# Optimization experiments

Measured on AMD Instinct MI355X. Metric: run time of the kernel, lower is better.

## Reference

```python
import jax, jax.numpy as jnp
import numpy as np
from jax.ops import segment_sum

GRID = 32        # cells per axis; offset grid is (GRID+1)^3
T = 48           # number of accepted MC topologies
N_PTS = 131072

# 12 cube edges: base (lower) corner offset and axis the edge runs along.
# e0..3: x/y edges of z=0 face, e4..7: same at z=1, e8..11: vertical z edges.
EDGE_BASE = np.array([[0,0,0],[1,0,0],[0,1,0],[0,0,0],
                      [0,0,1],[1,0,1],[0,1,1],[0,0,1],
                      [0,0,0],[1,0,0],[1,1,0],[0,1,0]], dtype=np.int32)
EDGE_AXIS = np.array([0,1,0,1, 0,1,0,1, 2,2,2,2], dtype=np.int32)
EDGE_DIR  = np.eye(3, dtype=np.float32)[EDGE_AXIS]          # [12,3] unit dirs


def _dot(u, v):
    return jnp.sum(u * v, axis=-1)


def _safe_div(n, d, eps=1e-12):
    return n / jnp.where(jnp.abs(d) > eps, d, eps)


def _point_tri_dist_sq(p, a, b, c):
    """Squared distance from p to triangle (a,b,c); Ericson closest-point
    algorithm with full vertex/edge/interior region clamping, vectorized.
    p broadcasts against a/b/c over leading dims; last dim is xyz."""
    ab = b - a; ac = c - a; ap = p - a
    d1 = _dot(ab, ap); d2 = _dot(ac, ap)
    bp = p - b; d3 = _dot(ab, bp); d4 = _dot(ac, bp)
    cp = p - c; d5 = _dot(ab, cp); d6 = _dot(ac, cp)
    vc = d1 * d4 - d3 * d2
    vb = d5 * d2 - d1 * d6
    va = d3 * d6 - d5 * d4
    v_ab = _safe_div(d1, d1 - d3)
    w_ac = _safe_div(d2, d2 - d6)
    w_bc = _safe_div(d4 - d3, (d4 - d3) + (d5 - d6))
    inv = _safe_div(jnp.ones_like(va), va + vb + vc)
    v_in = vb * inv; w_in = vc * inv
    q = a + ab * v_in[..., None] + ac * w_in[..., None]                      # interior
    q = jnp.where(((va <= 0) & ((d4 - d3) >= 0) & ((d5 - d6) >= 0))[..., None],
                  b + (c - b) * w_bc[..., None], q)                          # edge BC
    q = jnp.where(((vb <= 0) & (d2 >= 0) & (d6 <= 0))[..., None],
                  a + ac * w_ac[..., None], q)                               # edge AC
    q = jnp.where(((d6 >= 0) & (d5 <= d6))[..., None], c, q)                 # vertex C
    q = jnp.where(((vc <= 0) & (d1 >= 0) & (d3 <= 0))[..., None],
                  a + ab * v_ab[..., None], q)                               # edge AB
    q = jnp.where(((d3 >= 0) & (d4 <= d3))[..., None], b, q)                 # vertex B
    q = jnp.where(((d1 <= 0) & (d2 <= 0))[..., None], a, q)                  # vertex A
    diff = p - q
    return _dot(diff, diff)


def setup_inputs() -> dict:
    key = jax.random.key(0)
    k1, k2, k3 = jax.random.split(key, 3)
    offset = jax.random.uniform(k1, (3, GRID + 1, GRID + 1, GRID + 1), dtype=jnp.float32)
    points = jax.random.uniform(k2, (N_PTS, 3), dtype=jnp.float32) * GRID
    tri_table = jax.random.randint(k3, (T, 3, 3), 0, 12, dtype=jnp.int32)
    return {"offset": offset, "points": points, "tri_table": tri_table}


def reference(offset, points, tri_table):
    edge_base_i = jnp.asarray(EDGE_BASE)                 # [12,3] int
    edge_base_f = jnp.asarray(EDGE_BASE, dtype=offset.dtype)
    edge_dir = jnp.asarray(EDGE_DIR, dtype=offset.dtype)
    edge_axis = jnp.asarray(EDGE_AXIS)

    cell = jnp.clip(jnp.floor(points).astype(jnp.int32), 0, GRID - 1)   # [N,3]
    local = points - cell.astype(points.dtype)                          # [N,3] in [0,1)^3

    # grid index of each edge's base corner -> edge offset parameter t in [0,1]
    gidx = cell[:, None, :] + edge_base_i[None, :, :]                   # [N,12,3]
    t = offset[edge_axis[None, :], gidx[..., 0], gidx[..., 1], gidx[..., 2]]  # [N,12]
    verts = edge_base_f[None] + edge_dir[None] * t[..., None]           # [N,12,3] local coords

    tri = verts[:, tri_table]                                           # [N,T,3tri,3vert,3]
    a = tri[:, :, :, 0, :]; b = tri[:, :, :, 1, :]; c = tri[:, :, :, 2, :]
    p = local[:, None, None, :]                                         # [N,1,1,3]
    d2 = _point_tri_dist_sq(p, a, b, c)                                 # [N,T,3]
    d_min = jnp.min(d2, axis=-1)                                        # [N,T]

    cell_id = (cell[:, 0] * GRID + cell[:, 1]) * GRID + cell[:, 2]      # [N]
    distances_full = segment_sum(d_min, cell_id, num_segments=GRID ** 3)  # [GRID^3, T]
    return distances_full
```

## Files before the change

kernel.cpp:

```cpp
#include <hip/hip_runtime.h>

#define GRID 32
#define NT 48
#define BLK 256
#define SPLIT 16
#define PPB (BLK / SPLIT)
#define NCELLS (GRID * GRID * GRID)
#define CAP 32
#define CAP2 16
#define GSTRIDE 148

#define EDGE_PACK ( (0ULL<<0) | (9ULL<<5) | (2ULL<<10) | (8ULL<<15) | \
                    (4ULL<<20) | (13ULL<<25) | (6ULL<<30) | (12ULL<<35) | \
                    (16ULL<<40) | (17ULL<<45) | (19ULL<<50) | (18ULL<<55) )

__device__ __forceinline__ float tri_dist_gram(float AA, float AB, float AC,
                                               float BB, float BC, float CC) {
    float d1 = AA - AB, d2 = AA - AC;
    float d3 = AB - BB, d4 = AB - BC;
    float d5 = AC - BC, d6 = AC - CC;
    float d43 = BB - BC;
    float d56 = CC - BC;
    float vc = d1 * d4 - d3 * d2;
    float vb = d5 * d2 - d1 * d6;
    float va = d3 * d6 - d5 * d4;

    bool cbc = (va <= 0.f) & (d43 >= 0.f) & (d56 >= 0.f);
    bool cac = (vb <= 0.f) & (d2 >= 0.f) & (d6 <= 0.f);
    bool ccc = (d6 >= 0.f) & (d5 <= d6);
    bool cab = (vc <= 0.f) & (d1 >= 0.f) & (d3 <= 0.f);
    bool cbb = (d3 >= 0.f) & (d4 <= d3);
    bool caa = (d1 <= 0.f) & (d2 <= 0.f);

    float nv = vb, nw = vc, den = va + vb + vc;
    nw = cbc ? d43 : nw;  den = cbc ? d43 + d56 : den;
    nv = cac ? 0.f : nv;  nw = cac ? d2  : nw;  den = cac ? d2 - d6 : den;
    nv = cab ? d1  : nv;  nw = cab ? 0.f : nw;  den = cab ? d1 - d3 : den;
    bool mode = cbc & !cac & !cab;

    float dd  = (fabsf(den) > 1e-12f) ? den : 1e-12f;
    float inv = __builtin_amdgcn_rcpf(dd);
    float vp = nv * inv;
    float wp = nw * inv;
    float u = mode ? 0.f : 1.f - vp - wp;
    float v = mode ? 1.f - wp : vp;
    float e1 = fmaf(AC, wp, fmaf(AB, v, AA * u));
    float e2 = fmaf(BC, wp, fmaf(BB, v, AB * u));
    float e3 = fmaf(CC, wp, fmaf(BC, v, AC * u));
    float r  = fmaf(wp, e3, fmaf(v, e2, u * e1));
    r = (ccc & !cab) ? CC : r;
    r = cbb ? BB : r;
    r = caa ? AA : r;
    return r;
}

template<bool SLOT>
__global__ __launch_bounds__(BLK, 8) void eval_kernel(
    const float* __restrict__ offset,
    const float* __restrict__ points,
    const int*   __restrict__ tri_table,
    int*         __restrict__ cnt,
    int*         __restrict__ wlist,
    int*         __restrict__ ovf_cnt,
    int*         __restrict__ ovf,
    float*       __restrict__ dmin,
    float*       __restrict__ dmin_ovf,
    int n)
{
    __shared__ float4 v_s[PPB * 13];
    __shared__ float  gram[PPB * GSTRIDE];
    __shared__ int2   goff[NT * 3];
    __shared__ int    pos_s[PPB];

    const int tid = threadIdx.x;
    const int g   = blockIdx.x * BLK + tid;
    const int pt  = g >> 4;
    const int grp = tid & 15;
    const int pl  = tid >> 4;
    const bool active = (pt < n);

    if (tid < NT * 3) {
        int i = tri_table[tid * 3 + 0];
        int j = tri_table[tid * 3 + 1];
        int k = tri_table[tid * 3 + 2];
        int o0 = (i * 13) | ((i * 12 + j) << 8) | ((i * 12 + k) << 16);
        int o1 = (j * 13) | ((j * 12 + k) << 8) | ((k * 13) << 16);
        goff[tid] = make_int2(o0, o1);
    }

    float4 vi = make_float4(0.f, 0.f, 0.f, 0.f);
    if (active) {
        float px = points[pt * 3 + 0];
        float py = points[pt * 3 + 1];
        float pz = points[pt * 3 + 2];
        int cx = min(max((int)floorf(px), 0), GRID - 1);
        int cy = min(max((int)floorf(py), 0), GRID - 1);
        int cz = min(max((int)floorf(pz), 0), GRID - 1);
        if (grp == 0) {
            int cellid = ((cx * GRID) + cy) * GRID + cz;
            int pos = atomicAdd(&cnt[cellid], 1);
            if (SLOT) {
                int base;
                if (pos < CAP2) base = cellid * CAP2 + pos;
                else { int e = atomicAdd(ovf_cnt, 1); ovf[e] = cellid;
                       base = 0x40000000 | e; }
                pos_s[pl] = base;
            } else {
                if (pos < CAP) wlist[cellid * CAP + pos] = pt;
                else { int e = atomicAdd(ovf_cnt, 1); ovf[e] = (cellid << 17) | pt; }
            }
        }
        if (grp < 12) {
            float lx = px - (float)cx;
            float ly = py - (float)cy;
            float lz = pz - (float)cz;
            unsigned nib = (unsigned)(EDGE_PACK >> (5 * grp)) & 31u;
            int gx = cx + (int)(nib & 1u);
            int gy = cy + (int)((nib >> 1) & 1u);
            int gz = cz + (int)((nib >> 2) & 1u);
            int ax = (int)(nib >> 3);
            float t = offset[((ax * 33 + gx) * 33 + gy) * 33 + gz];
            float vx = (ax == 0) ? t : (float)(nib & 1u);
            float vy = (ax == 1) ? t : (float)((nib >> 1) & 1u);
            float vz = (ax == 2) ? t : (float)((nib >> 2) & 1u);
            vi = make_float4(lx - vx, ly - vy, lz - vz, 0.0f);
            v_s[pl * 13 + grp] = vi;
        }
    }
    __syncthreads();
    if (active && grp < 12) {
        float* gp = &gram[pl * GSTRIDE];
        int j = grp;
#pragma unroll
        for (int d = 0; d < 7; d++) {
            float4 vj = v_s[pl * 13 + j];
            float dv = fmaf(vi.z, vj.z, fmaf(vi.y, vj.y, vi.x * vj.x));
            gp[grp * 12 + j] = dv;
            gp[j * 12 + grp] = dv;
            j = (j == 11) ? 0 : j + 1;
        }
    }
    __syncthreads();
    if (!active) return;

    const float* gp = &gram[pl * GSTRIDE];
    const int2* gofft = &goff[grp * 9];
    float dm[3];
#pragma unroll
    for (int r = 0; r < 3; r++) {
        int2 oa = gofft[r * 3 + 0];
        int2 ob = gofft[r * 3 + 1];
        int2 oc = gofft[r * 3 + 2];
        float a0 = gp[oa.x & 255], a1 = gp[(oa.x >> 8) & 255], a2 = gp[(unsigned)oa.x >> 16];
        float a3 = gp[oa.y & 255], a4 = gp[(oa.y >> 8) & 255], a5 = gp[(unsigned)oa.y >> 16];
        float b0 = gp[ob.x & 255], b1 = gp[(ob.x >> 8) & 255], b2 = gp[(unsigned)ob.x >> 16];
        float b3 = gp[ob.y & 255], b4 = gp[(ob.y >> 8) & 255], b5 = gp[(unsigned)ob.y >> 16];
        float c0 = gp[oc.x & 255], c1 = gp[(oc.x >> 8) & 255], c2 = gp[(unsigned)oc.x >> 16];
        float c3 = gp[oc.y & 255], c4 = gp[(oc.y >> 8) & 255], c5 = gp[(unsigned)oc.y >> 16];
        float d0 = tri_dist_gram(a0, a1, a2, a3, a4, a5);
        float d1 = tri_dist_gram(b0, b1, b2, b3, b4, b5);
        float d2 = tri_dist_gram(c0, c1, c2, c3, c4, c5);
        dm[r] = fminf(fminf(d0, d1), d2);
    }
    float* dp;
    if (SLOT) {
        int base = pos_s[pl];
        dp = (base & 0x40000000)
               ? &dmin_ovf[(size_t)(base & 0x3FFFFFFF) * NT + grp * 3]
               : &dmin[(size_t)base * NT + grp * 3];
    } else {
        dp = &dmin[(size_t)pt * NT + grp * 3];
    }
    dp[0] = dm[0]; dp[1] = dm[1]; dp[2] = dm[2];
}

__global__ __launch_bounds__(BLK) void reduce_slot_kernel(
    const int*   __restrict__ cnt,
    const int*   __restrict__ ovf_cnt,
    const int*   __restrict__ ovf,
    const float* __restrict__ dmin,
    const float* __restrict__ dmin_ovf,
    float*       __restrict__ out)
{
    const int tid  = threadIdx.x;
    const int grp  = tid & 15;
    const int pl   = tid >> 4;
    const int cell = blockIdx.x * PPB + pl;

    const int c = min(cnt[cell], CAP2);
    const float* bp = &dmin[(size_t)cell * CAP2 * NT + grp * 3];
    float s0 = 0.f, s1 = 0.f, s2 = 0.f;
    for (int i = 0; i < c; i++) {
        s0 += bp[0]; s1 += bp[1]; s2 += bp[2];
        bp += NT;
    }
    const int movf = *ovf_cnt;
    for (int e = 0; e < movf; e++) {
        if (ovf[e] == cell) {
            const float* dp = &dmin_ovf[(size_t)e * NT + grp * 3];
            s0 += dp[0]; s1 += dp[1]; s2 += dp[2];
        }
    }
    float* op = &out[cell * NT + grp * 3];
    op[0] = s0; op[1] = s1; op[2] = s2;
}

__global__ __launch_bounds__(BLK) void reduce_kernel(
    const int*   __restrict__ cnt,
    const int*   __restrict__ wlist,
    const int*   __restrict__ ovf_cnt,
    const int*   __restrict__ ovf,
    const float* __restrict__ dmin,
    float*       __restrict__ out)
{
    const int tid  = threadIdx.x;
    const int grp  = tid & 15;
    const int pl   = tid >> 4;
    const int cell = blockIdx.x * PPB + pl;

    const int c = min(cnt[cell], CAP);
    const int* wl = &wlist[cell * CAP];
    float s0 = 0.f, s1 = 0.f, s2 = 0.f;
    for (int i = 0; i < c; i++) {
        int pt = wl[i];
        const float* dp = &dmin[(size_t)pt * NT + grp * 3];
        s0 += dp[0]; s1 += dp[1]; s2 += dp[2];
    }
    const int movf = *ovf_cnt;
    for (int e = 0; e < movf; e++) {
        int v = ovf[e];
        if ((v >> 17) == cell) {
            int pt = v & 0x1FFFF;
            const float* dp = &dmin[(size_t)pt * NT + grp * 3];
            s0 += dp[0]; s1 += dp[1]; s2 += dp[2];
        }
    }
    float* op = &out[cell * NT + grp * 3];
    op[0] = s0; op[1] = s1; op[2] = s2;
}

__global__ __launch_bounds__(BLK) void ptd_kernel(
    const float* __restrict__ offset,
    const float* __restrict__ points,
    const int*   __restrict__ tri_table,
    float*       __restrict__ out,
    int n)
{
    __shared__ float4 v_s[PPB * 13];
    __shared__ float  gram[PPB * GSTRIDE];
    __shared__ int2   goff[NT * 3];

    const int tid = threadIdx.x;
    const int g   = blockIdx.x * BLK + tid;
    const int pt  = g >> 4;
    const int grp = tid & 15;
    const int pl  = tid >> 4;
    const bool active = (pt < n);

    if (tid < NT * 3) {
        int i = tri_table[tid * 3 + 0];
        int j = tri_table[tid * 3 + 1];
        int k = tri_table[tid * 3 + 2];
        int o0 = (i * 13) | ((i * 12 + j) << 8) | ((i * 12 + k) << 16);
        int o1 = (j * 13) | ((j * 12 + k) << 8) | ((k * 13) << 16);
        goff[tid] = make_int2(o0, o1);
    }

    float4 vi = make_float4(0.f, 0.f, 0.f, 0.f);
    int cx = 0, cy = 0, cz = 0;
    if (active) {
        float px = points[pt * 3 + 0];
        float py = points[pt * 3 + 1];
        float pz = points[pt * 3 + 2];
        cx = min(max((int)floorf(px), 0), GRID - 1);
        cy = min(max((int)floorf(py), 0), GRID - 1);
        cz = min(max((int)floorf(pz), 0), GRID - 1);
        if (grp < 12) {
            float lx = px - (float)cx;
            float ly = py - (float)cy;
            float lz = pz - (float)cz;
            unsigned nib = (unsigned)(EDGE_PACK >> (5 * grp)) & 31u;
            int gx = cx + (int)(nib & 1u);
            int gy = cy + (int)((nib >> 1) & 1u);
            int gz = cz + (int)((nib >> 2) & 1u);
            int ax = (int)(nib >> 3);
            float t = offset[((ax * 33 + gx) * 33 + gy) * 33 + gz];
            float vx = (ax == 0) ? t : (float)(nib & 1u);
            float vy = (ax == 1) ? t : (float)((nib >> 1) & 1u);
            float vz = (ax == 2) ? t : (float)((nib >> 2) & 1u);
            vi = make_float4(lx - vx, ly - vy, lz - vz, 0.0f);
            v_s[pl * 13 + grp] = vi;
        }
    }
    __syncthreads();
    if (active && grp < 12) {
        float* gp = &gram[pl * GSTRIDE];
        int j = grp;
#pragma unroll
        for (int d = 0; d < 7; d++) {
            float4 vj = v_s[pl * 13 + j];
            float dv = fmaf(vi.z, vj.z, fmaf(vi.y, vj.y, vi.x * vj.x));
            gp[grp * 12 + j] = dv;
            gp[j * 12 + grp] = dv;
            j = (j == 11) ? 0 : j + 1;
        }
    }
    __syncthreads();
    if (!active) return;

    const float* gp = &gram[pl * GSTRIDE];
    float* outp = out + ((((cx * GRID) + cy) * GRID + cz) * NT);
    const int2* gofft = &goff[grp * 9];
#pragma unroll
    for (int r = 0; r < 3; r++) {
        float dmn;
#pragma unroll
        for (int k = 0; k < 3; k++) {
            int2 o = gofft[r * 3 + k];
            float AA = gp[o.x & 255];
            float AB = gp[(o.x >> 8) & 255];
            float AC = gp[(unsigned)o.x >> 16];
            float BB = gp[o.y & 255];
            float BC = gp[(o.y >> 8) & 255];
            float CC = gp[(unsigned)o.y >> 16];
            float d = tri_dist_gram(AA, AB, AC, BB, BC, CC);
            dmn = (k == 0) ? d : fminf(dmn, d);
        }
        atomicAdd(&outp[grp * 3 + r], dmn);
    }
}

extern "C" void kernel_launch(void* const* d_in, const int* in_sizes, int n_in,
                              void* d_out, int out_size, void* d_ws, size_t ws_size,
                              hipStream_t stream) {
    const float* offset    = (const float*)d_in[0];
    const float* points    = (const float*)d_in[1];
    const int*   tri_table = (const int*)d_in[2];
    float* out = (float*)d_out;
    int n = in_sizes[1] / 3;

    const size_t CNT_BYTES = (size_t)NCELLS * 4;
    const size_t OVFC_OFF  = CNT_BYTES;
    const size_t OVF_OFF   = CNT_BYTES + 128;
    const size_t TAIL_OFF  = (OVF_OFF + (size_t)n * 4 + 255) & ~(size_t)255;

    const size_t DMIN2_BYTES = (size_t)NCELLS * CAP2 * NT * 4;
    const size_t DOVF_OFF    = TAIL_OFF + DMIN2_BYTES;
    const size_t WS_SLOT     = DOVF_OFF + (size_t)n * NT * 4;

    const size_t WL_BYTES = (size_t)NCELLS * CAP * 4;
    const size_t DMIN_OFF = TAIL_OFF + WL_BYTES;
    const size_t WS_FB    = DMIN_OFF + (size_t)n * NT * 4;

    char* ws = (char*)d_ws;
    int* cnt     = (int*)(ws);
    int* ovf_cnt = (int*)(ws + OVFC_OFF);
    int* ovf     = (int*)(ws + OVF_OFF);

    long total = (long)n * SPLIT;
    int blocks = (int)((total + BLK - 1) / BLK);

    if (ws_size >= WS_SLOT) {
        float* dmin2    = (float*)(ws + TAIL_OFF);
        float* dmin_ovf = (float*)(ws + DOVF_OFF);
        hipMemsetAsync(ws, 0, OVF_OFF, stream);
        eval_kernel<true><<<blocks, BLK, 0, stream>>>(
            offset, points, tri_table, cnt, nullptr, ovf_cnt, ovf,
            dmin2, dmin_ovf, n);
        reduce_slot_kernel<<<NCELLS / PPB, BLK, 0, stream>>>(
            cnt, ovf_cnt, ovf, dmin2, dmin_ovf, out);
    } else if (ws_size >= WS_FB) {
        int*   wlist = (int*)(ws + TAIL_OFF);
        float* dmin  = (float*)(ws + DMIN_OFF);
        hipMemsetAsync(ws, 0, OVF_OFF, stream);
        eval_kernel<false><<<blocks, BLK, 0, stream>>>(
            offset, points, tri_table, cnt, wlist, ovf_cnt, ovf,
            dmin, nullptr, n);
        reduce_kernel<<<NCELLS / PPB, BLK, 0, stream>>>(
            cnt, wlist, ovf_cnt, ovf, dmin, out);
    } else {
        hipMemsetAsync(d_out, 0, (size_t)out_size * sizeof(float), stream);
        ptd_kernel<<<blocks, BLK, 0, stream>>>(offset, points, tri_table, out, n);
    }
}
```

Measured before the change: 112.6 us.

## Pack Gram matrix as float2 pairs to halve LDS reads per triangle

Stores the per-point Gram matrix interleaved as (G[i][j], G[j][j]) float2 pairs so each triangle needs three 8-byte LDS reads instead of six scalar reads. The offset table is repacked into one int per triangle and read as int4 rows. The aim is to cut LDS load instruction count in the hot evaluation loop. In exchange the shared-memory footprint roughly doubles and launch_bounds drops from 8 to 6 blocks, which may lower occupancy.

Result: no change. 112.3 us (-0.3%).

```diff
diff --git a/kernel.cpp b/kernel.cpp
--- a/kernel.cpp
+++ b/kernel.cpp
@@ -8,7 +8,10 @@
 #define NCELLS (GRID * GRID * GRID)
 #define CAP 32
 #define CAP2 16
-#define GSTRIDE 148
+#define GSTRIDE 144
+#define G2F 290
+
+typedef float f32x2 __attribute__((ext_vector_type(2)));
 
 #define EDGE_PACK ( (0ULL<<0) | (9ULL<<5) | (2ULL<<10) | (8ULL<<15) | \
                     (4ULL<<20) | (13ULL<<25) | (6ULL<<30) | (12ULL<<35) | \
@@ -54,8 +57,22 @@
     return r;
 }
 
+__device__ __forceinline__ float eval_one(const f32x2* gp2, int o) {
+    f32x2 pij = gp2[o & 255];
+    f32x2 pjk = gp2[(o >> 8) & 255];
+    f32x2 pki = gp2[(unsigned)o >> 16];
+    return tri_dist_gram(pij.y, pij.x, pki.x, pjk.y, pjk.x, pki.y);
+}
+
+__device__ __forceinline__ float row_min(const f32x2* gp2, int o0, int o1, int o2) {
+    float a = eval_one(gp2, o0);
+    float b = eval_one(gp2, o1);
+    float c = eval_one(gp2, o2);
+    return fminf(fminf(a, b), c);
+}
+
 template<bool SLOT>
-__global__ __launch_bounds__(BLK, 8) void eval_kernel(
+__global__ __launch_bounds__(BLK, 6) void eval_kernel(
     const float* __restrict__ offset,
     const float* __restrict__ points,
     const int*   __restrict__ tri_table,
@@ -68,8 +85,8 @@
     int n)
 {
     __shared__ float4 v_s[PPB * 13];
-    __shared__ float  gram[PPB * GSTRIDE];
-    __shared__ int2   goff[NT * 3];
+    __shared__ float  gram[PPB * G2F];
+    __shared__ int4   gtab4[16 * 3];
     __shared__ int    pos_s[PPB];
 
     const int tid = threadIdx.x;
@@ -83,9 +100,10 @@
         int i = tri_table[tid * 3 + 0];
         int j = tri_table[tid * 3 + 1];
         int k = tri_table[tid * 3 + 2];
-        int o0 = (i * 13) | ((i * 12 + j) << 8) | ((i * 12 + k) << 16);
-        int o1 = (j * 13) | ((j * 12 + k) << 8) | ((k * 13) << 16);
-        goff[tid] = make_int2(o0, o1);
+        int t  = tid / 3;
+        int kk = tid - t * 3;
+        int o = (i * 12 + j) | ((j * 12 + k) << 8) | ((k * 12 + i) << 16);
+        ((int*)gtab4)[(t / 3) * 12 + (t % 3) * 4 + kk] = o;
     }
 
     float4 vi = make_float4(0.f, 0.f, 0.f, 0.f);
@@ -129,39 +147,36 @@
     }
     __syncthreads();
     if (active && grp < 12) {
-        float* gp = &gram[pl * GSTRIDE];
-        int j = grp;
-#pragma unroll
-        for (int d = 0; d < 7; d++) {
+        float* gp = &gram[pl * G2F];
+        float diag = fmaf(vi.z, vi.z, fmaf(vi.y, vi.y, vi.x * vi.x));
+        *(f32x2*)&gp[2 * (grp * 13)] = (f32x2){diag, diag};
+        int j = (grp == 11) ? 0 : grp + 1;
+#pragma unroll
+        for (int d = 1; d < 7; d++) {
             float4 vj = v_s[pl * 13 + j];
             float dv = fmaf(vi.z, vj.z, fmaf(vi.y, vj.y, vi.x * vj.x));
-            gp[grp * 12 + j] = dv;
-            gp[j * 12 + grp] = dv;
+            *(f32x2*)&gp[2 * (grp * 12 + j)] = (f32x2){dv, diag};
+            gp[2 * (j * 12 + grp)] = dv;
+            j = (j == 11) ? 0 : j + 1;
+        }
+#pragma unroll
+        for (int d = 7; d < 12; d++) {
+            gp[2 * (grp * 12 + j) + 1] = diag;
             j = (j == 11) ? 0 : j + 1;
         }
     }
     __syncthreads();
     if (!active) return;
 
-    const float* gp = &gram[pl * GSTRIDE];
-    const int2* gofft = &goff[grp * 9];
-    float dm[3];
-#pragma unroll
-    for (int r = 0; r < 3; r++) {
-        int2 oa = gofft[r * 3 + 0];
-        int2 ob = gofft[r * 3 + 1];
-        int2 oc = gofft[r * 3 + 2];
-        float a0 = gp[oa.x & 255], a1 = gp[(oa.x >> 8) & 255], a2 = gp[(unsigned)oa.x >> 16];
-        float a3 = gp[oa.y & 255], a4 = gp[(oa.y >> 8) & 255], a5 = gp[(unsigned)oa.y >> 16];
-        float b0 = gp[ob.x & 255], b1 = gp[(ob.x >> 8) & 255], b2 = gp[(unsigned)ob.x >> 16];
-        float b3 = gp[ob.y & 255], b4 = gp[(ob.y >> 8) & 255], b5 = gp[(unsigned)ob.y >> 16];
-        float c0 = gp[oc.x & 255], c1 = gp[(oc.x >> 8) & 255], c2 = gp[(unsigned)oc.x >> 16];
-        float c3 = gp[oc.y & 255], c4 = gp[(oc.y >> 8) & 255], c5 = gp[(unsigned)oc.y >> 16];
-        float d0 = tri_dist_gram(a0, a1, a2, a3, a4, a5);
-        float d1 = tri_dist_gram(b0, b1, b2, b3, b4, b5);
-        float d2 = tri_dist_gram(c0, c1, c2, c3, c4, c5);
-        dm[r] = fminf(fminf(d0, d1), d2);
-    }
+    const f32x2* gp2 = (const f32x2*)&gram[pl * G2F];
+    const int4* gq = &gtab4[grp * 3];
+    int4 q0 = gq[0];
+    int4 q1 = gq[1];
+    int4 q2 = gq[2];
+    float dm0 = row_min(gp2, q0.x, q0.y, q0.z);
+    float dm1 = row_min(gp2, q1.x, q1.y, q1.z);
+    float dm2 = row_min(gp2, q2.x, q2.y, q2.z);
+
     float* dp;
     if (SLOT) {
         int base = pos_s[pl];
@@ -171,7 +186,7 @@
     } else {
         dp = &dmin[(size_t)pt * NT + grp * 3];
     }
-    dp[0] = dm[0]; dp[1] = dm[1]; dp[2] = dm[2];
+    dp[0] = dm0; dp[1] = dm1; dp[2] = dm2;
 }
 
 __global__ __launch_bounds__(BLK) void reduce_slot_kernel(
@@ -261,9 +276,8 @@
         int i = tri_table[tid * 3 + 0];
         int j = tri_table[tid * 3 + 1];
         int k = tri_table[tid * 3 + 2];
-        int o0 = (i * 13) | ((i * 12 + j) << 8) | ((i * 12 + k) << 16);
-        int o1 = (j * 13) | ((j * 12 + k) << 8) | ((k * 13) << 16);
-        goff[tid] = make_int2(o0, o1);
+        goff[tid] = make_int2((i * 13) | ((i * 12 + j) << 8) | ((i * 12 + k) << 16),
+                              (j * 13) | ((j * 12 + k) << 8) | ((k * 13) << 16));
     }
 
     float4 vi = make_float4(0.f, 0.f, 0.f, 0.f);
```
